# Performance work log

Hardware: AMD Instinct MI355X
Metric: run time of the kernel (lower is better)

## Reference

```python
import jax, jax.numpy as jnp
import numpy as np

N_FILTERS = 64
COV_EPS = 1e-4
ALPHA = 0.1  # cov_shrinkage_alpha

_tri_r, _tri_c = np.triu_indices(N_FILTERS)
_TRI_R = jnp.asarray(_tri_r)
_TRI_C = jnp.asarray(_tri_c)
_TRI_SCALE = jnp.where(_TRI_R != _TRI_C, np.sqrt(2.0), 1.0).astype(jnp.float32)


def setup_inputs() -> dict:
    key = jax.random.key(0)
    k1, k2 = jax.random.split(key)
    x = jax.random.normal(k1, (256, 128, 1, 4096), dtype=jnp.float32)
    # 1x1 conv weight [out_ch, in_ch] (kernel spatial dims are 1x1)
    proj_w = jax.random.normal(k2, (64, 128), dtype=jnp.float32) * 0.05
    return {"x": x, "proj_w": proj_w}


def reference(x, proj_w):
    # 1x1 conv channel projection: [B, Cin, 1, T] -> [B, F, T]
    x = jnp.einsum('bcht,fc->bfht', x, proj_w)[:, :, 0, :].astype(jnp.float32)
    # center over time
    x = x - x.mean(axis=-1, keepdims=True)
    denom = float(max(x.shape[-1] - 1, 1))
    cov = jnp.einsum('bft,bgt->bfg', x, x) / denom  # [B, F, F]
    n = cov.shape[-1]
    eye = jnp.eye(n, dtype=cov.dtype)
    # shrinkage toward scaled identity
    mu = jnp.trace(cov, axis1=-2, axis2=-1) / n  # [B]
    cov = (1.0 - ALPHA) * cov + ALPHA * mu[:, None, None] * eye
    # symmetrize + jitter
    cov = 0.5 * (cov + jnp.swapaxes(cov, -1, -2)) + COV_EPS * eye
    # log-Euclidean map via batched eigh
    eigvals, eigvecs = jnp.linalg.eigh(cov)
    eigvals = jnp.clip(eigvals, COV_EPS)
    log_cov = jnp.einsum('bij,bj,bkj->bik', eigvecs, jnp.log(eigvals), eigvecs)
    log_cov = 0.5 * (log_cov + jnp.swapaxes(log_cov, -1, -2))
    # upper-triangular vectorization with sqrt(2) off-diagonal scaling
    vec = log_cov[:, _TRI_R, _TRI_C] * _TRI_SCALE  # [B, F*(F+1)/2]
    return vec
```

## Files before the change

kernel.cpp:

```cpp
#include <hip/hip_runtime.h>

typedef __attribute__((ext_vector_type(8))) short s8_t;
typedef __attribute__((ext_vector_type(4))) float f4_t;

#define NBATCH 256
#define NCH    128
#define NT     4096
#define NF     64
#define TT     128
#define NIT    (NT / TT)
#define LDSK   (TT + 8)
#define CHEB_D 28

static __device__ __forceinline__ unsigned short f32_bf16(float f) {
    unsigned int u = __float_as_uint(f);
    return (unsigned short)((u + 0x7FFFu + ((u >> 16) & 1u)) >> 16);
}
static __device__ __forceinline__ float bf16_f32(unsigned short h) {
    return __uint_as_float(((unsigned int)h) << 16);
}

__global__ __launch_bounds__(256, 1)
void k_gram(const float* __restrict__ x, float* __restrict__ gws, float* __restrict__ sxws) {
    __shared__ __align__(16) unsigned short xl[2][NCH * LDSK];
    __shared__ float red[256];

    const int tid  = threadIdx.x;
    const int b    = blockIdx.x;
    const int lane = tid & 63;
    const int wv   = tid >> 6;
    const int lrow8  = tid >> 5;
    const int lchunk = tid & 31;

    const float* xb = x + (size_t)b * ((size_t)NCH * NT);

    f4_t acc[2][8];
    #pragma unroll
    for (int i = 0; i < 2; ++i)
        #pragma unroll
        for (int j = 0; j < 8; ++j)
            acc[i][j] = (f4_t){0.f, 0.f, 0.f, 0.f};

    float sxp = 0.f;
    float4 ld[16];

    #pragma unroll
    for (int j = 0; j < 16; ++j) {
        const int r = j * 8 + lrow8;
        ld[j] = *(const float4*)(xb + (size_t)r * NT + lchunk * 4);
    }
    #pragma unroll
    for (int j = 0; j < 16; ++j) {
        const int r = j * 8 + lrow8;
        ushort4 h;
        h.x = f32_bf16(ld[j].x); h.y = f32_bf16(ld[j].y);
        h.z = f32_bf16(ld[j].z); h.w = f32_bf16(ld[j].w);
        *(ushort4*)&xl[0][r * LDSK + lchunk * 4] = h;
    }
    __syncthreads();

    for (int it = 0; it < NIT; ++it) {
        const int cur = it & 1;
        if (it + 1 < NIT) {
            const int t0 = (it + 1) * TT;
            #pragma unroll
            for (int j = 0; j < 16; ++j) {
                const int r = j * 8 + lrow8;
                ld[j] = *(const float4*)(xb + (size_t)r * NT + t0 + lchunk * 4);
            }
        }
        const unsigned short* bufc = xl[cur];
        {
            const int lrow = lane & 15;
            const int koff = (lane >> 4) * 8;
            #pragma unroll
            for (int ks = 0; ks < TT / 32; ++ks) {
                const int k0 = ks * 32 + koff;
                s8_t bf[8];
                #pragma unroll
                for (int cb = 0; cb < 8; ++cb)
                    bf[cb] = *(const s8_t*)&bufc[(cb * 16 + lrow) * LDSK + k0];
                #pragma unroll
                for (int i = 0; i < 2; ++i) {
                    const s8_t af = *(const s8_t*)&bufc[((wv * 2 + i) * 16 + lrow) * LDSK + k0];
                    #pragma unroll
                    for (int cb = 0; cb < 8; ++cb)
                        acc[i][cb] = __builtin_amdgcn_mfma_f32_16x16x32_bf16(af, bf[cb], acc[i][cb], 0, 0, 0);
                }
            }
        }
        {
            const unsigned short* rp = &bufc[(tid >> 1) * LDSK + (tid & 1) * 64];
            float s = 0.f;
            #pragma unroll
            for (int q8 = 0; q8 < 8; ++q8) {
                s8_t v = *(const s8_t*)&rp[q8 * 8];
                #pragma unroll
                for (int e = 0; e < 8; ++e)
                    s += bf16_f32((unsigned short)v[e]);
            }
            sxp += s;
        }
        if (it + 1 < NIT) {
            #pragma unroll
            for (int j = 0; j < 16; ++j) {
                const int r = j * 8 + lrow8;
                ushort4 h;
                h.x = f32_bf16(ld[j].x); h.y = f32_bf16(ld[j].y);
                h.z = f32_bf16(ld[j].z); h.w = f32_bf16(ld[j].w);
                *(ushort4*)&xl[cur ^ 1][r * LDSK + lchunk * 4] = h;
            }
        }
        __syncthreads();
    }

    float* gb = gws + ((size_t)b << 14);
    const int lrow4 = (lane >> 4) * 4;
    const int lcol  = lane & 15;
    #pragma unroll
    for (int i = 0; i < 2; ++i) {
        const int rbase = (wv * 2 + i) * 16 + lrow4;
        #pragma unroll
        for (int cb = 0; cb < 8; ++cb) {
            const int col = cb * 16 + lcol;
            #pragma unroll
            for (int reg = 0; reg < 4; ++reg)
                gb[(size_t)(rbase + reg) * NCH + col] = acc[i][cb][reg];
        }
    }
    red[tid] = sxp;
    __syncthreads();
    if (tid < NCH)
        sxws[b * NCH + tid] = red[2 * tid] + red[2 * tid + 1];
}

__global__ __launch_bounds__(256, 1)
void k_logm(const float* __restrict__ gws, const float* __restrict__ sxws,
            const float* __restrict__ wmat, float* __restrict__ out) {
    __shared__ __align__(16) float lds[33032];
    float* sG   = lds;
    float* sC0  = lds;
    float* sU   = lds;
    float* sB0  = lds + 4096;
    float* sB1  = lds + 8192;
    float* sA   = lds + 12288;
    float* sWt  = lds + 16384;
    float* sM1t = lds + 24576;
    float* ssx  = lds + 32768;
    float* sp   = lds + 32896;
    float* sred = lds + 32960;
    float* sscal= lds + 33024;

    const int tid = threadIdx.x;
    const int b   = blockIdx.x;

    for (int i = tid; i < NF * NCH; i += 256) {
        const int k = i >> 6, f = i & 63;
        sWt[i] = wmat[f * NCH + k];
    }
    if (tid < NCH) ssx[tid] = sxws[b * NCH + tid];
    {
        const float* gb = gws + ((size_t)b << 14);
        for (int i = tid; i < NCH * NCH; i += 256) sG[i] = gb[i];
    }
    __syncthreads();

    {
        const int f0 = (tid >> 4) * 4, c0 = (tid & 15) * 8;
        float a[4][8];
        #pragma unroll
        for (int i = 0; i < 4; ++i)
            #pragma unroll
            for (int j = 0; j < 8; ++j) a[i][j] = 0.f;
        for (int k = 0; k < NCH; ++k) {
            const float4 wv4 = *(const float4*)&sWt[k * 64 + f0];
            const float4 gA  = *(const float4*)&sG[k * NCH + c0];
            const float4 gB  = *(const float4*)&sG[k * NCH + c0 + 4];
            const float wa[4] = {wv4.x, wv4.y, wv4.z, wv4.w};
            const float ga[8] = {gA.x, gA.y, gA.z, gA.w, gB.x, gB.y, gB.z, gB.w};
            #pragma unroll
            for (int i = 0; i < 4; ++i)
                #pragma unroll
                for (int j = 0; j < 8; ++j)
                    a[i][j] = fmaf(wa[i], ga[j], a[i][j]);
        }
        #pragma unroll
        for (int j = 0; j < 8; ++j) {
            float4 v; v.x = a[0][j]; v.y = a[1][j]; v.z = a[2][j]; v.w = a[3][j];
            *(float4*)&sM1t[(c0 + j) * 64 + f0] = v;
        }
    }
    if (tid < NF) {
        float s = 0.f;
        for (int k = 0; k < NCH; ++k) s = fmaf(sWt[k * 64 + tid], ssx[k], s);
        sp[tid] = s;
    }
    __syncthreads();

    {
        const int f0 = (tid >> 4) * 4, g0 = (tid & 15) * 4;
        float a[4][4];
        #pragma unroll
        for (int i = 0; i < 4; ++i)
            #pragma unroll
            for (int j = 0; j < 4; ++j) a[i][j] = 0.f;
        for (int k = 0; k < NCH; ++k) {
            const float4 mv = *(const float4*)&sM1t[k * 64 + f0];
            const float4 wv4 = *(const float4*)&sWt[k * 64 + g0];
            const float ma[4] = {mv.x, mv.y, mv.z, mv.w};
            const float wa[4] = {wv4.x, wv4.y, wv4.z, wv4.w};
            #pragma unroll
            for (int i = 0; i < 4; ++i)
                #pragma unroll
                for (int j = 0; j < 4; ++j)
                    a[i][j] = fmaf(ma[i], wa[j], a[i][j]);
        }
        const float i4096 = 1.f / 4096.f, i4095 = 1.f / 4095.f;
        #pragma unroll
        for (int i = 0; i < 4; ++i)
            #pragma unroll
            for (int j = 0; j < 4; ++j)
                sC0[(f0 + i) * 64 + (g0 + j)] =
                    (a[i][j] - sp[f0 + i] * sp[g0 + j] * i4096) * i4095;
    }
    __syncthreads();

    if (tid == 0) {
        float s = 0.f;
        for (int i = 0; i < 64; ++i) s += sC0[i * 65];
        sscal[0] = s * (1.f / 64.f);
    }
    __syncthreads();

    const float mu = sscal[0];
    const float dshift = 0.1f * mu + 1e-4f;
    for (int i = tid; i < 4096; i += 256) {
        const int r = i >> 6, c = i & 63;
        float v = 0.45f * (sC0[r * 64 + c] + sC0[c * 64 + r]);
        if (r == c) v += dshift;
        sA[i] = v;
    }
    __syncthreads();

    if (tid < 64) {
        float s = 0.f;
        for (int j = 0; j < 64; ++j) s += fabsf(sA[j * 64 + tid]);
        sred[tid] = s;
    }
    __syncthreads();
    if (tid == 0) {
        float hi = 0.f;
        for (int i = 0; i < 64; ++i) hi = fmaxf(hi, sred[i]);
        const float lo = dshift;
        hi = fmaxf(hi, lo * 1.02f);
        float wsc = (hi - lo) / (hi + lo);
        wsc = fminf(fmaxf(wsc, 1e-6f), 0.999999f);
        const float zz = fmaxf((1.f - sqrtf(fmaxf(1.f - wsc * wsc, 1e-12f))) / wsc, 1e-12f);
        const float mc = 0.5f * (hi + lo);
        sscal[1] = mc;
        sscal[2] = wsc;
        sscal[3] = zz;
        sscal[4] = logf(mc) - log1pf(zz * zz);
    }
    __syncthreads();

    {
        const float mc = sscal[1], wsc = sscal[2];
        const float inv_mw = 1.f / (mc * wsc);
        const float inv_w  = 1.f / wsc;
        for (int i = tid; i < 4096; i += 256) {
            const int r = i >> 6, c = i & 63;
            float v = sA[i] * inv_mw;
            if (r == c) v -= inv_w;
            sU[i] = v;
        }
    }
    __syncthreads();

    const int f0 = (tid >> 4) * 4, g0 = (tid & 15) * 4;
    const float zc  = sscal[3];
    const float l2z = log2f(zc);
    float rP[4][4], rP2[4][4];
    {
        const float cd = 2.f * ((CHEB_D & 1) ? 1.f : -1.f) *
                         exp2f((float)CHEB_D * l2z) / (float)CHEB_D;
        #pragma unroll
        for (int i = 0; i < 4; ++i)
            #pragma unroll
            for (int j = 0; j < 4; ++j) {
                rP[i][j]  = (f0 + i == g0 + j) ? cd : 0.f;
                rP2[i][j] = 0.f;
            }
        #pragma unroll
        for (int i = 0; i < 4; ++i) {
            float4 v; v.x = rP[i][0]; v.y = rP[i][1]; v.z = rP[i][2]; v.w = rP[i][3];
            *(float4*)&sB0[(f0 + i) * 64 + g0] = v;
        }
    }
    __syncthreads();

    float* bcur = sB0;
    float* bnxt = sB1;
    for (int k = CHEB_D - 1; k >= 1; --k) {
        const float ck = 2.f * ((k & 1) ? 1.f : -1.f) * exp2f((float)k * l2z) / (float)k;
        float a[4][4];
        #pragma unroll
        for (int i = 0; i < 4; ++i)
            #pragma unroll
            for (int j = 0; j < 4; ++j) a[i][j] = 0.f;
        for (int kk = 0; kk < 64; ++kk) {
            const float4 uv = *(const float4*)&sU[kk * 64 + f0];
            const float4 bv = *(const float4*)&bcur[kk * 64 + g0];
            const float ua[4] = {uv.x, uv.y, uv.z, uv.w};
            const float ba[4] = {bv.x, bv.y, bv.z, bv.w};
            #pragma unroll
            for (int i = 0; i < 4; ++i)
                #pragma unroll
                for (int j = 0; j < 4; ++j)
                    a[i][j] = fmaf(ua[i], ba[j], a[i][j]);
        }
        #pragma unroll
        for (int i = 0; i < 4; ++i)
            #pragma unroll
            for (int j = 0; j < 4; ++j) {
                const float v = 2.f * a[i][j] - rP2[i][j] + ((f0 + i == g0 + j) ? ck : 0.f);
                rP2[i][j] = rP[i][j];
                rP[i][j]  = v;
            }
        #pragma unroll
        for (int i = 0; i < 4; ++i) {
            float4 v; v.x = rP[i][0]; v.y = rP[i][1]; v.z = rP[i][2]; v.w = rP[i][3];
            *(float4*)&bnxt[(f0 + i) * 64 + g0] = v;
        }
        float* t = bcur; bcur = bnxt; bnxt = t;
        __syncthreads();
    }
    {
        const float c0c = sscal[4];
        float a[4][4];
        #pragma unroll
        for (int i = 0; i < 4; ++i)
            #pragma unroll
            for (int j = 0; j < 4; ++j) a[i][j] = 0.f;
        for (int kk = 0; kk < 64; ++kk) {
            const float4 uv = *(const float4*)&sU[kk * 64 + f0];
            const float4 bv = *(const float4*)&bcur[kk * 64 + g0];
            const float ua[4] = {uv.x, uv.y, uv.z, uv.w};
            const float ba[4] = {bv.x, bv.y, bv.z, bv.w};
            #pragma unroll
            for (int i = 0; i < 4; ++i)
                #pragma unroll
                for (int j = 0; j < 4; ++j)
                    a[i][j] = fmaf(ua[i], ba[j], a[i][j]);
        }
        #pragma unroll
        for (int i = 0; i < 4; ++i) {
            float4 v;
            float vv[4];
            #pragma unroll
            for (int j = 0; j < 4; ++j)
                vv[j] = ((f0 + i == g0 + j) ? c0c : 0.f) + a[i][j] - rP2[i][j];
            v.x = vv[0]; v.y = vv[1]; v.z = vv[2]; v.w = vv[3];
            *(float4*)&bnxt[(f0 + i) * 64 + g0] = v;
        }
    }
    __syncthreads();
    const float* sF = bnxt;

    float* ob = out + (size_t)b * 2080;
    for (int idx = tid; idx < 2080; idx += 256) {
        const double disc = 16641.0 - 8.0 * (double)idx;
        const int i = (int)((129.0 - sqrt(disc)) * 0.5);
        const int Si = i * 64 - (i * (i - 1)) / 2;
        const int j = i + (idx - Si);
        float v = 0.5f * (sF[i * 64 + j] + sF[j * 64 + i]);
        if (i != j) v *= 1.4142135623730951f;
        ob[idx] = v;
    }
}

extern "C" void kernel_launch(void* const* d_in, const int* in_sizes, int n_in,
                              void* d_out, int out_size, void* d_ws, size_t ws_size,
                              hipStream_t stream) {
    const float* x    = (const float*)d_in[0];
    const float* wmat = (const float*)d_in[1];
    float* outp = (float*)d_out;
    float* gws  = (float*)d_ws;
    float* sxws = gws + (size_t)NBATCH * NCH * NCH;
    k_gram<<<dim3(NBATCH), dim3(256), 0, stream>>>(x, gws, sxws);
    k_logm<<<dim3(NBATCH), dim3(256), 0, stream>>>(gws, sxws, wmat, outp);
}
```

Before: 777.6 us.

## Split Gram over time chunks, widen blocks to 512 threads, cut Chebyshev degree

The Gram kernel now splits the time axis into four chunks, each handled by its own 512-thread block, which gives 1024 blocks instead of 256 and writes partial Gram matrices and sums to workspace. The logm kernel adds the four partials together, uses 512 threads with smaller per-thread tiles, and transposes the weights through LDS. The Chebyshev degree for the matrix log drops from 28 to 20, which reduces the serial matmul iterations but may lose accuracy. The aims are better CU utilisation and latency hiding on a memory-bound Gram pass, at the cost of extra workspace traffic.

Measured after the change: 780.1 us. No clear change (+0.3%).

```diff
diff --git a/kernel.cpp b/kernel.cpp
--- a/kernel.cpp
+++ b/kernel.cpp
@@ -8,9 +8,11 @@
 #define NT     4096
 #define NF     64
 #define TT     128
-#define NIT    (NT / TT)
+#define CHUNKS 4
+#define CT     (NT / CHUNKS)
+#define NIT    (CT / TT)
 #define LDSK   (TT + 8)
-#define CHEB_D 28
+#define CHEB_D 20
 
 static __device__ __forceinline__ unsigned short f32_bf16(float f) {
     unsigned int u = __float_as_uint(f);
@@ -20,38 +22,45 @@
     return __uint_as_float(((unsigned int)h) << 16);
 }
 
-__global__ __launch_bounds__(256, 1)
+__global__ __launch_bounds__(512, 4)
 void k_gram(const float* __restrict__ x, float* __restrict__ gws, float* __restrict__ sxws) {
     __shared__ __align__(16) unsigned short xl[2][NCH * LDSK];
-    __shared__ float red[256];
+    __shared__ float red[512];
 
     const int tid  = threadIdx.x;
-    const int b    = blockIdx.x;
     const int lane = tid & 63;
     const int wv   = tid >> 6;
-    const int lrow8  = tid >> 5;
+    const int bid  = blockIdx.x;
+    const int b    = bid >> 2;
+    const int chnk = bid & 3;
+    const int lrow16 = tid >> 5;
     const int lchunk = tid & 31;
 
-    const float* xb = x + (size_t)b * ((size_t)NCH * NT);
-
-    f4_t acc[2][8];
+    const float* xb = x + (size_t)b * ((size_t)NCH * NT) + chnk * CT;
+
+    const int arow0 = (wv & 3) * 32;
+    const int bcol0 = (wv >> 2) * 64;
+    const int lrow  = lane & 15;
+    const int koff  = (lane >> 4) * 8;
+
+    f4_t acc[2][4];
     #pragma unroll
     for (int i = 0; i < 2; ++i)
         #pragma unroll
-        for (int j = 0; j < 8; ++j)
+        for (int j = 0; j < 4; ++j)
             acc[i][j] = (f4_t){0.f, 0.f, 0.f, 0.f};
 
     float sxp = 0.f;
-    float4 ld[16];
+    float4 ld[8];
 
     #pragma unroll
-    for (int j = 0; j < 16; ++j) {
-        const int r = j * 8 + lrow8;
+    for (int j = 0; j < 8; ++j) {
+        const int r = j * 16 + lrow16;
         ld[j] = *(const float4*)(xb + (size_t)r * NT + lchunk * 4);
     }
     #pragma unroll
-    for (int j = 0; j < 16; ++j) {
-        const int r = j * 8 + lrow8;
+    for (int j = 0; j < 8; ++j) {
+        const int r = j * 16 + lrow16;
         ushort4 h;
         h.x = f32_bf16(ld[j].x); h.y = f32_bf16(ld[j].y);
         h.z = f32_bf16(ld[j].z); h.w = f32_bf16(ld[j].w);
@@ -64,37 +73,30 @@
         if (it + 1 < NIT) {
             const int t0 = (it + 1) * TT;
             #pragma unroll
-            for (int j = 0; j < 16; ++j) {
-                const int r = j * 8 + lrow8;
+            for (int j = 0; j < 8; ++j) {
+                const int r = j * 16 + lrow16;
                 ld[j] = *(const float4*)(xb + (size_t)r * NT + t0 + lchunk * 4);
             }
         }
         const unsigned short* bufc = xl[cur];
+        #pragma unroll
+        for (int ks = 0; ks < TT / 32; ++ks) {
+            const int k0 = ks * 32 + koff;
+            const s8_t af0 = *(const s8_t*)&bufc[(arow0 + lrow) * LDSK + k0];
+            const s8_t af1 = *(const s8_t*)&bufc[(arow0 + 16 + lrow) * LDSK + k0];
+            #pragma unroll
+            for (int cb = 0; cb < 4; ++cb) {
+                const s8_t bf = *(const s8_t*)&bufc[(bcol0 + cb * 16 + lrow) * LDSK + k0];
+                acc[0][cb] = __builtin_amdgcn_mfma_f32_16x16x32_bf16(af0, bf, acc[0][cb], 0, 0, 0);
+                acc[1][cb] = __builtin_amdgcn_mfma_f32_16x16x32_bf16(af1, bf, acc[1][cb], 0, 0, 0);
+            }
+        }
         {
-            const int lrow = lane & 15;
-            const int koff = (lane >> 4) * 8;
-            #pragma unroll
-            for (int ks = 0; ks < TT / 32; ++ks) {
-                const int k0 = ks * 32 + koff;
-                s8_t bf[8];
-                #pragma unroll
-                for (int cb = 0; cb < 8; ++cb)
-                    bf[cb] = *(const s8_t*)&bufc[(cb * 16 + lrow) * LDSK + k0];
-                #pragma unroll
-                for (int i = 0; i < 2; ++i) {
-                    const s8_t af = *(const s8_t*)&bufc[((wv * 2 + i) * 16 + lrow) * LDSK + k0];
-                    #pragma unroll
-                    for (int cb = 0; cb < 8; ++cb)
-                        acc[i][cb] = __builtin_amdgcn_mfma_f32_16x16x32_bf16(af, bf[cb], acc[i][cb], 0, 0, 0);
-                }
-            }
-        }
-        {
-            const unsigned short* rp = &bufc[(tid >> 1) * LDSK + (tid & 1) * 64];
+            const unsigned short* rp = &bufc[(tid >> 2) * LDSK + (tid & 3) * 32];
             float s = 0.f;
             #pragma unroll
-            for (int q8 = 0; q8 < 8; ++q8) {
-                s8_t v = *(const s8_t*)&rp[q8 * 8];
+            for (int q = 0; q < 4; ++q) {
+                s8_t v = *(const s8_t*)&rp[q * 8];
                 #pragma unroll
                 for (int e = 0; e < 8; ++e)
                     s += bf16_f32((unsigned short)v[e]);
@@ -103,8 +105,8 @@
         }
         if (it + 1 < NIT) {
             #pragma unroll
-            for (int j = 0; j < 16; ++j) {
-                const int r = j * 8 + lrow8;
+            for (int j = 0; j < 8; ++j) {
+                const int r = j * 16 + lrow16;
                 ushort4 h;
                 h.x = f32_bf16(ld[j].x); h.y = f32_bf16(ld[j].y);
                 h.z = f32_bf16(ld[j].z); h.w = f32_bf16(ld[j].w);
@@ -114,15 +116,15 @@
         __syncthreads();
     }
 
-    float* gb = gws + ((size_t)b << 14);
+    float* gb = gws + ((size_t)bid << 14);
     const int lrow4 = (lane >> 4) * 4;
     const int lcol  = lane & 15;
     #pragma unroll
     for (int i = 0; i < 2; ++i) {
-        const int rbase = (wv * 2 + i) * 16 + lrow4;
-        #pragma unroll
-        for (int cb = 0; cb < 8; ++cb) {
-            const int col = cb * 16 + lcol;
+        const int rbase = arow0 + i * 16 + lrow4;
+        #pragma unroll
+        for (int cb = 0; cb < 4; ++cb) {
+            const int col = bcol0 + cb * 16 + lcol;
             #pragma unroll
             for (int reg = 0; reg < 4; ++reg)
                 gb[(size_t)(rbase + reg) * NCH + col] = acc[i][cb][reg];
@@ -131,19 +133,18 @@
     red[tid] = sxp;
     __syncthreads();
     if (tid < NCH)
-        sxws[b * NCH + tid] = red[2 * tid] + red[2 * tid + 1];
-}
-
-__global__ __launch_bounds__(256, 1)
+        sxws[bid * NCH + tid] = red[tid * 4] + red[tid * 4 + 1] + red[tid * 4 + 2] + red[tid * 4 + 3];
+}
+
+__global__ __launch_bounds__(512, 2)
 void k_logm(const float* __restrict__ gws, const float* __restrict__ sxws,
             const float* __restrict__ wmat, float* __restrict__ out) {
     __shared__ __align__(16) float lds[33032];
     float* sG   = lds;
     float* sC0  = lds;
-    float* sU   = lds;
-    float* sB0  = lds + 4096;
-    float* sB1  = lds + 8192;
-    float* sA   = lds + 12288;
+    float* sU   = lds + 4096;
+    float* sB0  = lds + 8192;
+    float* sB1  = lds + 12288;
     float* sWt  = lds + 16384;
     float* sM1t = lds + 24576;
     float* ssx  = lds + 32768;
@@ -154,38 +155,54 @@
     const int tid = threadIdx.x;
     const int b   = blockIdx.x;
 
-    for (int i = tid; i < NF * NCH; i += 256) {
-        const int k = i >> 6, f = i & 63;
-        sWt[i] = wmat[f * NCH + k];
-    }
-    if (tid < NCH) ssx[tid] = sxws[b * NCH + tid];
-    {
-        const float* gb = gws + ((size_t)b << 14);
-        for (int i = tid; i < NCH * NCH; i += 256) sG[i] = gb[i];
-    }
-    __syncthreads();
-
-    {
-        const int f0 = (tid >> 4) * 4, c0 = (tid & 15) * 8;
-        float a[4][8];
+    for (int i = tid; i < NF * NCH; i += 512) sM1t[i] = wmat[i];
+    if (tid < NCH) {
+        const float* sxb = sxws + (size_t)b * 4 * NCH;
+        ssx[tid] = sxb[tid] + sxb[NCH + tid] + sxb[2 * NCH + tid] + sxb[3 * NCH + tid];
+    }
+    {
+        const float4* g0 = (const float4*)(gws + ((size_t)(b * 4 + 0) << 14));
+        const float4* g1 = (const float4*)(gws + ((size_t)(b * 4 + 1) << 14));
+        const float4* g2 = (const float4*)(gws + ((size_t)(b * 4 + 2) << 14));
+        const float4* g3 = (const float4*)(gws + ((size_t)(b * 4 + 3) << 14));
+        float4* dst = (float4*)sG;
+        for (int i = tid; i < 4096; i += 512) {
+            const float4 a = g0[i], c = g1[i], d = g2[i], e = g3[i];
+            float4 r;
+            r.x = a.x + c.x + d.x + e.x;
+            r.y = a.y + c.y + d.y + e.y;
+            r.z = a.z + c.z + d.z + e.z;
+            r.w = a.w + c.w + d.w + e.w;
+            dst[i] = r;
+        }
+    }
+    __syncthreads();
+    for (int i = tid; i < NF * NCH; i += 512) {
+        const int f = i >> 7, k = i & 127;
+        sWt[k * 64 + f] = sM1t[i];
+    }
+    __syncthreads();
+
+    {
+        const int f0 = (tid >> 5) * 4, c0 = (tid & 31) * 4;
+        float a[4][4];
         #pragma unroll
         for (int i = 0; i < 4; ++i)
             #pragma unroll
-            for (int j = 0; j < 8; ++j) a[i][j] = 0.f;
+            for (int j = 0; j < 4; ++j) a[i][j] = 0.f;
         for (int k = 0; k < NCH; ++k) {
-            const float4 wv4 = *(const float4*)&sWt[k * 64 + f0];
-            const float4 gA  = *(const float4*)&sG[k * NCH + c0];
-            const float4 gB  = *(const float4*)&sG[k * NCH + c0 + 4];
-            const float wa[4] = {wv4.x, wv4.y, wv4.z, wv4.w};
-            const float ga[8] = {gA.x, gA.y, gA.z, gA.w, gB.x, gB.y, gB.z, gB.w};
+            const float4 w4 = *(const float4*)&sWt[k * 64 + f0];
+            const float4 g4 = *(const float4*)&sG[k * NCH + c0];
+            const float wa[4] = {w4.x, w4.y, w4.z, w4.w};
+            const float ga[4] = {g4.x, g4.y, g4.z, g4.w};
             #pragma unroll
             for (int i = 0; i < 4; ++i)
                 #pragma unroll
-                for (int j = 0; j < 8; ++j)
+                for (int j = 0; j < 4; ++j)
                     a[i][j] = fmaf(wa[i], ga[j], a[i][j]);
         }
         #pragma unroll
-        for (int j = 0; j < 8; ++j) {
+        for (int j = 0; j < 4; ++j) {
             float4 v; v.x = a[0][j]; v.y = a[1][j]; v.z = a[2][j]; v.w = a[3][j];
             *(float4*)&sM1t[(c0 + j) * 64 + f0] = v;
         }
@@ -198,30 +215,27 @@
     __syncthreads();
 
     {
-        const int f0 = (tid >> 4) * 4, g0 = (tid & 15) * 4;
-        float a[4][4];
+        const int f0 = (tid >> 5) * 4, g2 = (tid & 31) * 2;
+        float a[4][2];
+        #pragma unroll
+        for (int i = 0; i < 4; ++i) { a[i][0] = 0.f; a[i][1] = 0.f; }
+        for (int k = 0; k < NCH; ++k) {
+            const float4 m4 = *(const float4*)&sM1t[k * 64 + f0];
+            const float2 w2 = *(const float2*)&sWt[k * 64 + g2];
+            const float ma[4] = {m4.x, m4.y, m4.z, m4.w};
+            #pragma unroll
+            for (int i = 0; i < 4; ++i) {
+                a[i][0] = fmaf(ma[i], w2.x, a[i][0]);
+                a[i][1] = fmaf(ma[i], w2.y, a[i][1]);
+            }
+        }
+        const float i4096 = 1.f / 4096.f, i4095 = 1.f / 4095.f;
         #pragma unroll
         for (int i = 0; i < 4; ++i)
             #pragma unroll
-            for (int j = 0; j < 4; ++j) a[i][j] = 0.f;
-        for (int k = 0; k < NCH; ++k) {
-            const float4 mv = *(const float4*)&sM1t[k * 64 + f0];
-            const float4 wv4 = *(const float4*)&sWt[k * 64 + g0];
-            const float ma[4] = {mv.x, mv.y, mv.z, mv.w};
-            const float wa[4] = {wv4.x, wv4.y, wv4.z, wv4.w};
-            #pragma unroll
-            for (int i = 0; i < 4; ++i)
-                #pragma unroll
-                for (int j = 0; j < 4; ++j)
-                    a[i][j] = fmaf(ma[i], wa[j], a[i][j]);
-        }
-        const float i4096 = 1.f / 4096.f, i4095 = 1.f / 4095.f;
-        #pragma unroll
-        for (int i = 0; i < 4; ++i)
-            #pragma unroll
-            for (int j = 0; j < 4; ++j)
-                sC0[(f0 + i) * 64 + (g0 + j)] =
-                    (a[i][j] - sp[f0 + i] * sp[g0 + j] * i4096) * i4095;
+            for (int j = 0; j < 2; ++j)
+                sC0[(f0 + i) * 64 + (g2 + j)] =
+                    (a[i][j] - sp[f0 + i] * sp[g2 + j] * i4096) * i4095;
     }
     __syncthreads();
 
@@ -234,17 +248,17 @@
 
     const float mu = sscal[0];
     const float dshift = 0.1f * mu + 1e-4f;
-    for (int i = tid; i < 4096; i += 256) {
+    for (int i = tid; i < 4096; i += 512) {
         const int r = i >> 6, c = i & 63;
         float v = 0.45f * (sC0[r * 64 + c] + sC0[c * 64 + r]);
         if (r == c) v += dshift;
-        sA[i] = v;
+        sU[i] = v;
     }
     __syncthreads();
 
     if (tid < 64) {
         float s = 0.f;
-        for (int j = 0; j < 64; ++j) s += fabsf(sA[j * 64 + tid]);
+        for (int j = 0; j < 64; ++j) s += fabsf(sU[j * 64 + tid]);
         sred[tid] = s;
     }
     __syncthreads();
@@ -268,33 +282,33 @@
         const float mc = sscal[1], wsc = sscal[2];
         const float inv_mw = 1.f / (mc * wsc);
         const float inv_w  = 1.f / wsc;
-        for (int i = tid; i < 4096; i += 256) {
+        for (int i = tid; i < 4096; i += 512) {
             const int r = i >> 6, c = i & 63;
-            float v = sA[i] * inv_mw;
+            float v = sU[i] * inv_mw;
             if (r == c) v -= inv_w;
             sU[i] = v;
         }
     }
     __syncthreads();
 
-    const int f0 = (tid >> 4) * 4, g0 = (tid & 15) * 4;
+    const int f0 = (tid >> 5) * 4, g2 = (tid & 31) * 2;
     const float zc  = sscal[3];
     const float l2z = log2f(zc);
-    float rP[4][4], rP2[4][4];
+    float rP[4][2], rP2[4][2];
     {
         const float cd = 2.f * ((CHEB_D & 1) ? 1.f : -1.f) *
                          exp2f((float)CHEB_D * l2z) / (float)CHEB_D;
         #pragma unroll
         for (int i = 0; i < 4; ++i)
             #pragma unroll
-            for (int j = 0; j < 4; ++j) {
-                rP[i][j]  = (f0 + i == g0 + j) ? cd : 0.f;
+            for (int j = 0; j < 2; ++j) {
+                rP[i][j]  = (f0 + i == g2 + j) ? cd : 0.f;
                 rP2[i][j] = 0.f;
             }
         #pragma unroll
         for (int i = 0; i < 4; ++i) {
-            float4 v; v.x = rP[i][0]; v.y = rP[i][1]; v.z = rP[i][2]; v.w = rP[i][3];
-            *(float4*)&sB0[(f0 + i) * 64 + g0] = v;
+            float2 v; v.x = rP[i][0]; v.y = rP[i][1];
+            *(float2*)&sB0[(f0 + i) * 64 + g2] = v;
         }
     }
     __syncthreads();
@@ -303,72 +317,65 @@
     float* bnxt = sB1;
     for (int k = CHEB_D - 1; k >= 1; --k) {
         const float ck = 2.f * ((k & 1) ? 1.f : -1.f) * exp2f((float)k * l2z) / (float)k;
-        float a[4][4];
+        float a[4][2];
+        #pragma unroll
+        for (int i = 0; i < 4; ++i) { a[i][0] = 0.f; a[i][1] = 0.f; }
+        #pragma unroll 4
+        for (int kk = 0; kk < 64; ++kk) {
+            const float4 u4 = *(const float4*)&sU[kk * 64 + f0];
+            const float2 b2 = *(const float2*)&bcur[kk * 64 + g2];
+            const float ua[4] = {u4.x, u4.y, u4.z, u4.w};
+            #pragma unroll
+            for (int i = 0; i < 4; ++i) {
+                a[i][0] = fmaf(ua[i], b2.x, a[i][0]);
+                a[i][1] = fmaf(ua[i], b2.y, a[i][1]);
+            }
+        }
         #pragma unroll
         for (int i = 0; i < 4; ++i)
             #pragma unroll
-            for (int j = 0; j < 4; ++j) a[i][j] = 0.f;
-        for (int kk = 0; kk < 64; ++kk) {
-            const float4 uv = *(const float4*)&sU[kk * 64 + f0];
-            const float4 bv = *(const float4*)&bcur[kk * 64 + g0];
-            const float ua[4] = {uv.x, uv.y, uv.z, uv.w};
-            const float ba[4] = {bv.x, bv.y, bv.z, bv.w};
-            #pragma unroll
-            for (int i = 0; i < 4; ++i)
-                #pragma unroll
-                for (int j = 0; j < 4; ++j)
-                    a[i][j] = fmaf(ua[i], ba[j], a[i][j]);
-        }
-        #pragma unroll
-        for (int i = 0; i < 4; ++i)
-            #pragma unroll
-            for (int j = 0; j < 4; ++j) {
-                const float v = 2.f * a[i][j] - rP2[i][j] + ((f0 + i == g0 + j) ? ck : 0.f);
+            for (int j = 0; j < 2; ++j) {
+                const float v = 2.f * a[i][j] - rP2[i][j] + ((f0 + i == g2 + j) ? ck : 0.f);
                 rP2[i][j] = rP[i][j];
                 rP[i][j]  = v;
             }
         #pragma unroll
         for (int i = 0; i < 4; ++i) {
-            float4 v; v.x = rP[i][0]; v.y = rP[i][1]; v.z = rP[i][2]; v.w = rP[i][3];
-            *(float4*)&bnxt[(f0 + i) * 64 + g0] = v;
+            float2 v; v.x = rP[i][0]; v.y = rP[i][1];
+            *(float2*)&bnxt[(f0 + i) * 64 + g2] = v;
         }
         float* t = bcur; bcur = bnxt; bnxt = t;
         __syncthreads();
     }
     {
         const float c0c = sscal[4];
-        float a[4][4];
-        #pragma unroll
-        for (int i = 0; i < 4; ++i)
-            #pragma unroll
-            for (int j = 0; j < 4; ++j) a[i][j] = 0.f;
+        float a[4][2];
+        #pragma unroll
+        for (int i = 0; i < 4; ++i) { a[i][0] = 0.f; a[i][1] = 0.f; }
+        #pragma unroll 4
         for (int kk = 0; kk < 64; ++kk) {
-            const float4 uv = *(const float4*)&sU[kk * 64 + f0];
-            const float4 bv = *(const float4*)&bcur[kk * 64 + g0];
-            const float ua[4] = {uv.x, uv.y, uv.z, uv.w};
-            const float ba[4] = {bv.x, bv.y, bv.z, bv.w};
-            #pragma unroll
-            for (int i = 0; i < 4; ++i)
-                #pragma unroll
-                for (int j = 0; j < 4; ++j)
-                    a[i][j] = fmaf(ua[i], ba[j], a[i][j]);
+            const float4 u4 = *(const float4*)&sU[kk * 64 + f0];
+            const float2 b2 = *(const float2*)&bcur[kk * 64 + g2];
+            const float ua[4] = {u4.x, u4.y, u4.z, u4.w};
+            #pragma unroll
+            for (int i = 0; i < 4; ++i) {
+                a[i][0] = fmaf(ua[i], b2.x, a[i][0]);
+                a[i][1] = fmaf(ua[i], b2.y, a[i][1]);
+            }
         }
         #pragma unroll
         for (int i = 0; i < 4; ++i) {
-            float4 v;
-            float vv[4];
-            #pragma unroll
-            for (int j = 0; j < 4; ++j)
-                vv[j] = ((f0 + i == g0 + j) ? c0c : 0.f) + a[i][j] - rP2[i][j];
-            v.x = vv[0]; v.y = vv[1]; v.z = vv[2]; v.w = vv[3];
-            *(float4*)&bnxt[(f0 + i) * 64 + g0] = v;
+            float2 v;
+            v.x = ((f0 + i == g2 + 0) ? c0c : 0.f) + a[i][0] - rP2[i][0];
+            v.y = ((f0 + i == g2 + 1) ? c0c : 0.f) + a[i][1] - rP2[i][1];
+            *(float2*)&bnxt[(f0 + i) * 64 + g2] = v;
         }
     }
     __syncthreads();
     const float* sF = bnxt;
 
     float* ob = out + (size_t)b * 2080;
-    for (int idx = tid; idx < 2080; idx += 256) {
+    for (int idx = tid; idx < 2080; idx += 512) {
         const double disc = 16641.0 - 8.0 * (double)idx;
         const int i = (int)((129.0 - sqrt(disc)) * 0.5);
         const int Si = i * 64 - (i * (i - 1)) / 2;
@@ -386,7 +393,7 @@
     const float* wmat = (const float*)d_in[1];
     float* outp = (float*)d_out;
     float* gws  = (float*)d_ws;
-    float* sxws = gws + (size_t)NBATCH * NCH * NCH;
-    k_gram<<<dim3(NBATCH), dim3(256), 0, stream>>>(x, gws, sxws);
-    k_logm<<<dim3(NBATCH), dim3(256), 0, stream>>>(gws, sxws, wmat, outp);
-}
+    float* sxws = gws + (size_t)NBATCH * CHUNKS * NCH * NCH;
+    k_gram<<<dim3(NBATCH * CHUNKS), dim3(512), 0, stream>>>(x, gws, sxws);
+    k_logm<<<dim3(NBATCH), dim3(512), 0, stream>>>(gws, sxws, wmat, outp);
+}
```
